# Performance work log

Hardware: AMD Instinct MI355X
Metric: run time of the kernel (lower is better)

The kernel has to match this reference:

```python
import jax, jax.numpy as jnp
import numpy as np

IN_DIM = 128
NODES = 512      # nodes per graph (equal-size graphs, as x.view(bsize,-1,in_dim) assumes)
BSIZE = 512
T = 10
ALPHA = 0.1
REG = 1e-3
EPS = 1e-5       # torch LayerNorm default eps


def _layernorm(h, g, b):
    m = jnp.mean(h, axis=-1, keepdims=True)
    v = jnp.var(h, axis=-1, keepdims=True)  # biased, like torch LayerNorm
    return (h - m) * jax.lax.rsqrt(v + EPS) * g + b


def setup_inputs() -> dict:
    key = jax.random.key(0)
    ks = jax.random.split(key, 12)
    d, h = IN_DIM, IN_DIM // 2
    x = jax.random.normal(ks[0], (BSIZE * NODES, d), dtype=jnp.float32)
    batch = jnp.repeat(jnp.arange(BSIZE, dtype=jnp.int64), NODES)
    def lin(k, fi, fo):
        bound = 1.0 / np.sqrt(fi)
        k1, k2 = jax.random.split(k)
        W = jax.random.uniform(k1, (fi, fo), jnp.float32, -bound, bound)
        b = jax.random.uniform(k2, (fo,), jnp.float32, -bound, bound)
        return W, b
    W1, b1 = lin(ks[1], 2 * d, d)
    W2, b2 = lin(ks[2], d, h)
    W3, b3 = lin(ks[3], h, 10)
    g1, be1 = jnp.ones((d,), jnp.float32), jnp.zeros((d,), jnp.float32)
    g2, be2 = jnp.ones((h,), jnp.float32), jnp.zeros((h,), jnp.float32)
    return {"x": x, "batch": batch, "W1": W1, "b1": b1, "g1": g1, "be1": be1,
            "W2": W2, "b2": b2, "g2": g2, "be2": be2, "W3": W3, "b3": b3}


def reference(x, batch, W1, b1, g1, be1, W2, b2, g2, be2, W3, b3):
    bsize = x.shape[0] // NODES  # batch ids are 0..bsize-1, NODES nodes per graph
    x3 = x.reshape(bsize, NODES, IN_DIM)

    def potential(z):  # z: [B, N, 2*d] -> [B, N, 10]
        hh = _layernorm(jnp.tanh(z @ W1 + b1), g1, be1)
        hh = _layernorm(jnp.tanh(hh @ W2 + b2), g2, be2)
        return hh @ W3 + b3

    def energy_sum(y):  # scalar: sum over graphs of per-graph energy
        yb = jnp.broadcast_to(y[:, None, :], x3.shape)
        p = potential(jnp.concatenate([x3, yb], axis=-1))
        u = jnp.mean(p * p, axis=-1).sum(axis=-1) + REG * jnp.mean(y * y, axis=-1)
        return u.sum()

    egrad = jax.grad(energy_sum)

    def step(y, _):
        g = egrad(y)
        return y - ALPHA * g, g

    y0 = jnp.zeros((bsize, IN_DIM), dtype=x.dtype)
    yT, grads = jax.lax.scan(step, y0, None, length=T)
    return yT, grads
```

## Files before the change

### kernel.cpp

```cpp
#include <hip/hip_runtime.h>


typedef __attribute__((ext_vector_type(8))) short s8v;
typedef __attribute__((ext_vector_type(4))) float f4v;

#define OFF_W1T 0
#define OFF_W1Y 67584
#define OFF_W2T 102400
#define OFF_W2B 118784
#define OFF_W3T 135168
#define OFF_W3B 137216
#define OFF_YBF 141312
#define OFF_YF  272384

static __device__ __forceinline__ unsigned short f2b(float f){
  unsigned u = __float_as_uint(f);
  u = u + 0x7FFFu + ((u >> 16) & 1u);
  return (unsigned short)(u >> 16);
}
static __device__ __forceinline__ float ftanh(float a){
  float e = __expf(2.0f * a);
  return 1.0f - __fdividef(2.0f, e + 1.0f);
}
static __device__ __forceinline__ float rsum16(float v){
  v += __shfl_xor(v, 1); v += __shfl_xor(v, 2);
  v += __shfl_xor(v, 4); v += __shfl_xor(v, 8);
  return v;
}
static __device__ __forceinline__ f4v mfma16(s8v a, s8v b, f4v c){
  return __builtin_amdgcn_mfma_f32_16x16x32_bf16(a, b, c, 0, 0, 0);
}

__global__ void prep_kernel(const float* __restrict__ W1, const float* __restrict__ W2,
                            const float* __restrict__ W3, char* __restrict__ ws){
  int tid = blockIdx.x * blockDim.x + threadIdx.x;
  int nt = gridDim.x * blockDim.x;
  unsigned short* w1t = (unsigned short*)(ws + OFF_W1T);
  for (int idx = tid; idx < 128 * 256; idx += nt){
    int n = idx >> 8, k = idx & 255;
    w1t[n * 264 + k] = f2b(W1[k * 128 + n]);
  }
  unsigned short* w1y = (unsigned short*)(ws + OFF_W1Y);
  for (int idx = tid; idx < 128 * 128; idx += nt){
    int n = idx >> 7, k = idx & 127;
    w1y[n * 136 + k] = f2b(W1[(128 + n) * 128 + k]);
  }
  unsigned short* w2t = (unsigned short*)(ws + OFF_W2T);
  for (int idx = tid; idx < 16 * 512; idx += nt){
    int f = idx >> 9, pos = idx & 511, l = pos >> 3, j = pos & 7;
    int ntile = f >> 2, kt = f & 3;
    int n = ntile * 16 + (l & 15), k = kt * 32 + (l >> 4) * 8 + j;
    w2t[idx] = f2b(W2[k * 64 + n]);
  }
  unsigned short* w2b = (unsigned short*)(ws + OFF_W2B);
  for (int idx = tid; idx < 16 * 512; idx += nt){
    int f = idx >> 9, pos = idx & 511, l = pos >> 3, j = pos & 7;
    int ntile = f >> 1, kt = f & 1;
    int n = ntile * 16 + (l & 15), k = kt * 32 + (l >> 4) * 8 + j;
    w2b[idx] = f2b(W2[n * 64 + k]);
  }
  unsigned short* w3t = (unsigned short*)(ws + OFF_W3T);
  for (int idx = tid; idx < 2 * 512; idx += nt){
    int f = idx >> 9, pos = idx & 511, l = pos >> 3, j = pos & 7;
    int n = (l & 15), k = f * 32 + (l >> 4) * 8 + j;
    w3t[idx] = (n < 10) ? f2b(W3[k * 10 + n]) : (unsigned short)0;
  }
  unsigned short* w3b = (unsigned short*)(ws + OFF_W3B);
  for (int idx = tid; idx < 4 * 512; idx += nt){
    int f = idx >> 9, pos = idx & 511, l = pos >> 3, j = pos & 7;
    int n = f * 16 + (l & 15), k = (l >> 4) * 8 + j;
    w3b[idx] = (k < 10) ? f2b(W3[n * 10 + k]) : (unsigned short)0;
  }
}

struct __align__(16) SMem {
  unsigned short w1t[128 * 264];
  unsigned short w1y[128 * 136];
  unsigned short buf1[64 * 136];
  unsigned short buf2[64 * 72];
  float red_s[64][4];
  float red_q[64][4];
  unsigned short ybuf[128];
};

__launch_bounds__(512, 2)
__global__ void node_kernel(const float* __restrict__ x,
    const float* __restrict__ b1, const float* __restrict__ g1, const float* __restrict__ be1,
    const float* __restrict__ b2, const float* __restrict__ g2, const float* __restrict__ be2,
    const float* __restrict__ b3,
    const char* __restrict__ ws, float* __restrict__ grads_t){
  __shared__ SMem sm;
  const int tid = threadIdx.x;
  const int lane = tid & 63;
  const int w  = tid >> 6;
  const int wm = w >> 2;
  const int wn = w & 3;
  const int lg = lane >> 4;
  const int lr = lane & 15;

  const unsigned short* w2t_g = (const unsigned short*)(ws + OFF_W2T);
  const unsigned short* w2b_g = (const unsigned short*)(ws + OFF_W2B);
  const unsigned short* w3t_g = (const unsigned short*)(ws + OFF_W3T);
  const unsigned short* w3b_g = (const unsigned short*)(ws + OFF_W3B);
  const unsigned short* ybf_g = (const unsigned short*)(ws + OFF_YBF);

  {
    const uint4* src = (const uint4*)(ws + OFF_W1T);
    uint4* dst = (uint4*)&sm.w1t[0];
    #pragma unroll 1
    for (int i = tid; i < (67584 + 34816) / 16; i += 512) dst[i] = src[i];
  }

  const f4v z4 = {0.f, 0.f, 0.f, 0.f};
  const s8v z8 = {0, 0, 0, 0, 0, 0, 0, 0};

  #pragma unroll 1
  for (int c = blockIdx.x; c < 4096; c += gridDim.x){
    const int graph = c >> 3;
    const int node0 = c << 6;
    if (tid < 16) ((uint4*)sm.ybuf)[tid] = ((const uint4*)(ybf_g + graph * 128))[tid];
    __syncthreads();

    f4v acc1[2][2];
    acc1[0][0]=z4; acc1[0][1]=z4; acc1[1][0]=z4; acc1[1][1]=z4;
    #pragma unroll
    for (int kt = 0; kt < 8; ++kt){
      s8v af[2];
      if (kt < 4){
        #pragma unroll
        for (int i = 0; i < 2; ++i){
          const float* p = x + (size_t)(node0 + (wm*2+i)*16 + lr) * 128 + kt*32 + lg*8;
          float4 f0 = *(const float4*)p;
          float4 f1 = *(const float4*)(p + 4);
          s8v t;
          t[0]=(short)f2b(f0.x); t[1]=(short)f2b(f0.y); t[2]=(short)f2b(f0.z); t[3]=(short)f2b(f0.w);
          t[4]=(short)f2b(f1.x); t[5]=(short)f2b(f1.y); t[6]=(short)f2b(f1.z); t[7]=(short)f2b(f1.w);
          af[i] = t;
        }
      } else {
        s8v t = *(const s8v*)&sm.ybuf[(kt-4)*32 + lg*8];
        af[0] = t; af[1] = t;
      }
      #pragma unroll
      for (int jn = 0; jn < 2; ++jn){
        s8v bf = *(const s8v*)&sm.w1t[((wn*2+jn)*16 + lr)*264 + kt*32 + lg*8];
        #pragma unroll
        for (int i = 0; i < 2; ++i)
          acc1[i][jn] = mfma16(af[i], bf, acc1[i][jn]);
      }
    }

    float tv[2][2][4], xh1[2][2][4], dd1[2][2][4], sig1[2][4];
    #pragma unroll
    for (int i = 0; i < 2; ++i)
      #pragma unroll
      for (int jn = 0; jn < 2; ++jn){
        float bb = b1[wn*32 + jn*16 + lr];
        #pragma unroll
        for (int r = 0; r < 4; ++r)
          tv[i][jn][r] = ftanh(acc1[i][jn][r] + bb);
      }
    #pragma unroll
    for (int i = 0; i < 2; ++i)
      #pragma unroll
      for (int r = 0; r < 4; ++r){
        float s = tv[i][0][r] + tv[i][1][r];
        float q = tv[i][0][r]*tv[i][0][r] + tv[i][1][r]*tv[i][1][r];
        s = rsum16(s); q = rsum16(q);
        if (lr == 0){
          int row = (wm*2+i)*16 + lg*4 + r;
          sm.red_s[row][wn] = s; sm.red_q[row][wn] = q;
        }
      }
    __syncthreads();
    #pragma unroll
    for (int i = 0; i < 2; ++i)
      #pragma unroll
      for (int r = 0; r < 4; ++r){
        int row = (wm*2+i)*16 + lg*4 + r;
        float4 ss = *(const float4*)&sm.red_s[row][0];
        float4 qq = *(const float4*)&sm.red_q[row][0];
        float S = (ss.x + ss.y) + (ss.z + ss.w);
        float Q = (qq.x + qq.y) + (qq.z + qq.w);
        float mu  = S * (1.0f/128.0f);
        float var = Q * (1.0f/128.0f) - mu*mu;
        float sg  = rsqrtf(var + 1e-5f);
        sig1[i][r] = sg;
        #pragma unroll
        for (int jn = 0; jn < 2; ++jn){
          int col = wn*32 + jn*16 + lr;
          float tt = tv[i][jn][r];
          float xh = (tt - mu) * sg;
          xh1[i][jn][r] = xh;
          dd1[i][jn][r] = 1.0f - tt*tt;
          sm.buf1[row*136 + col] = f2b(xh * g1[col] + be1[col]);
        }
      }
    __syncthreads();

    f4v acc2[2]; acc2[0]=z4; acc2[1]=z4;
    #pragma unroll
    for (int kt = 0; kt < 4; ++kt){
      s8v bf = *(const s8v*)(w2t_g + ((wn*4 + kt)*64 + lane)*8);
      #pragma unroll
      for (int i = 0; i < 2; ++i){
        s8v af = *(const s8v*)&sm.buf1[((wm*2+i)*16 + lr)*136 + kt*32 + lg*8];
        acc2[i] = mfma16(af, bf, acc2[i]);
      }
    }
    float t2[2][4], xh2[2][4], dd2[2][4], sig2[2][4];
    {
      const int col2 = wn*16 + lr;
      float bb = b2[col2];
      #pragma unroll
      for (int i = 0; i < 2; ++i)
        #pragma unroll
        for (int r = 0; r < 4; ++r)
          t2[i][r] = ftanh(acc2[i][r] + bb);
      #pragma unroll
      for (int i = 0; i < 2; ++i)
        #pragma unroll
        for (int r = 0; r < 4; ++r){
          float s = rsum16(t2[i][r]);
          float q = rsum16(t2[i][r]*t2[i][r]);
          if (lr == 0){
            int row = (wm*2+i)*16 + lg*4 + r;
            sm.red_s[row][wn] = s; sm.red_q[row][wn] = q;
          }
        }
      __syncthreads();
      #pragma unroll
      for (int i = 0; i < 2; ++i)
        #pragma unroll
        for (int r = 0; r < 4; ++r){
          int row = (wm*2+i)*16 + lg*4 + r;
          float4 ss = *(const float4*)&sm.red_s[row][0];
          float4 qq = *(const float4*)&sm.red_q[row][0];
          float S = (ss.x+ss.y)+(ss.z+ss.w);
          float Q = (qq.x+qq.y)+(qq.z+qq.w);
          float mu  = S * (1.0f/64.0f);
          float var = Q * (1.0f/64.0f) - mu*mu;
          float sg  = rsqrtf(var + 1e-5f);
          sig2[i][r] = sg;
          float tt = t2[i][r];
          float xh = (tt - mu) * sg;
          xh2[i][r] = xh; dd2[i][r] = 1.0f - tt*tt;
          sm.buf2[row*72 + col2] = f2b(xh * g2[col2] + be2[col2]);
        }
      __syncthreads();
    }

    if (wn == 0){
      f4v acc3[2]; acc3[0]=z4; acc3[1]=z4;
      #pragma unroll
      for (int kt = 0; kt < 2; ++kt){
        s8v bf = *(const s8v*)(w3t_g + (kt*64 + lane)*8);
        #pragma unroll
        for (int i = 0; i < 2; ++i){
          s8v af = *(const s8v*)&sm.buf2[((wm*2+i)*16 + lr)*72 + kt*32 + lg*8];
          acc3[i] = mfma16(af, bf, acc3[i]);
        }
      }
      float bb3 = (lr < 10) ? b3[lr] : 0.0f;
      #pragma unroll
      for (int i = 0; i < 2; ++i)
        #pragma unroll
        for (int r = 0; r < 4; ++r){
          int row = (wm*2+i)*16 + lg*4 + r;
          float p = acc3[i][r] + bb3;
          sm.buf1[row*24 + lr] = (lr < 10) ? f2b(0.2f * p) : (unsigned short)0;
        }
    }
    __syncthreads();

    f4v accb3[2]; accb3[0]=z4; accb3[1]=z4;
    {
      s8v bf = *(const s8v*)(w3b_g + (wn*64 + lane)*8);
      #pragma unroll
      for (int i = 0; i < 2; ++i){
        s8v af = z8;
        if (lg < 2) af = *(const s8v*)&sm.buf1[((wm*2+i)*16 + lr)*24 + lg*8];
        accb3[i] = mfma16(af, bf, accb3[i]);
      }
    }
    {
      const int col2 = wn*16 + lr;
      float gg = g2[col2];
      float dyv2[2][4];
      #pragma unroll
      for (int i = 0; i < 2; ++i)
        #pragma unroll
        for (int r = 0; r < 4; ++r){
          float dy = accb3[i][r] * gg;
          dyv2[i][r] = dy;
          float s1 = rsum16(dy);
          float s2 = rsum16(dy * xh2[i][r]);
          if (lr == 0){
            int row = (wm*2+i)*16 + lg*4 + r;
            sm.red_s[row][wn] = s1; sm.red_q[row][wn] = s2;
          }
        }
      __syncthreads();
      #pragma unroll
      for (int i = 0; i < 2; ++i)
        #pragma unroll
        for (int r = 0; r < 4; ++r){
          int row = (wm*2+i)*16 + lg*4 + r;
          float4 ss = *(const float4*)&sm.red_s[row][0];
          float4 qq = *(const float4*)&sm.red_q[row][0];
          float S1 = (ss.x+ss.y)+(ss.z+ss.w);
          float S2 = (qq.x+qq.y)+(qq.z+qq.w);
          float dt = sig2[i][r] * (dyv2[i][r] - S1*(1.0f/64.0f) - xh2[i][r]*S2*(1.0f/64.0f));
          sm.buf2[row*72 + col2] = f2b(dt * dd2[i][r]);
        }
      __syncthreads();
    }

    f4v accb2[2][2];
    accb2[0][0]=z4; accb2[0][1]=z4; accb2[1][0]=z4; accb2[1][1]=z4;
    #pragma unroll
    for (int kt = 0; kt < 2; ++kt){
      s8v af[2];
      #pragma unroll
      for (int i = 0; i < 2; ++i)
        af[i] = *(const s8v*)&sm.buf2[((wm*2+i)*16 + lr)*72 + kt*32 + lg*8];
      #pragma unroll
      for (int jn = 0; jn < 2; ++jn){
        s8v bf = *(const s8v*)(w2b_g + (((wn*2+jn)*2 + kt)*64 + lane)*8);
        #pragma unroll
        for (int i = 0; i < 2; ++i)
          accb2[i][jn] = mfma16(af[i], bf, accb2[i][jn]);
      }
    }
    {
      float dyv[2][2][4];
      #pragma unroll
      for (int i = 0; i < 2; ++i)
        #pragma unroll
        for (int jn = 0; jn < 2; ++jn){
          float gg = g1[wn*32 + jn*16 + lr];
          #pragma unroll
          for (int r = 0; r < 4; ++r)
            dyv[i][jn][r] = accb2[i][jn][r] * gg;
        }
      #pragma unroll
      for (int i = 0; i < 2; ++i)
        #pragma unroll
        for (int r = 0; r < 4; ++r){
          float s1 = dyv[i][0][r] + dyv[i][1][r];
          float s2 = dyv[i][0][r]*xh1[i][0][r] + dyv[i][1][r]*xh1[i][1][r];
          s1 = rsum16(s1); s2 = rsum16(s2);
          if (lr == 0){
            int row = (wm*2+i)*16 + lg*4 + r;
            sm.red_s[row][wn] = s1; sm.red_q[row][wn] = s2;
          }
        }
      __syncthreads();
      #pragma unroll
      for (int i = 0; i < 2; ++i)
        #pragma unroll
        for (int r = 0; r < 4; ++r){
          int row = (wm*2+i)*16 + lg*4 + r;
          float4 ss = *(const float4*)&sm.red_s[row][0];
          float4 qq = *(const float4*)&sm.red_q[row][0];
          float S1 = (ss.x+ss.y)+(ss.z+ss.w);
          float S2 = (qq.x+qq.y)+(qq.z+qq.w);
          #pragma unroll
          for (int jn = 0; jn < 2; ++jn){
            int col = wn*32 + jn*16 + lr;
            float dt = sig1[i][r]*(dyv[i][jn][r] - S1*(1.0f/128.0f) - xh1[i][jn][r]*S2*(1.0f/128.0f));
            sm.buf1[row*136 + col] = f2b(dt * dd1[i][jn][r]);
          }
        }
      __syncthreads();
    }

    f4v accz[2][2];
    accz[0][0]=z4; accz[0][1]=z4; accz[1][0]=z4; accz[1][1]=z4;
    #pragma unroll
    for (int kt = 0; kt < 4; ++kt){
      s8v af[2];
      #pragma unroll
      for (int i = 0; i < 2; ++i)
        af[i] = *(const s8v*)&sm.buf1[((wm*2+i)*16 + lr)*136 + kt*32 + lg*8];
      #pragma unroll
      for (int jn = 0; jn < 2; ++jn){
        s8v bf = *(const s8v*)&sm.w1y[((wn*2+jn)*16 + lr)*136 + kt*32 + lg*8];
        #pragma unroll
        for (int i = 0; i < 2; ++i)
          accz[i][jn] = mfma16(af[i], bf, accz[i][jn]);
      }
    }
    #pragma unroll
    for (int jn = 0; jn < 2; ++jn){
      float s = ((accz[0][jn][0] + accz[0][jn][1]) + (accz[0][jn][2] + accz[0][jn][3]))
              + ((accz[1][jn][0] + accz[1][jn][1]) + (accz[1][jn][2] + accz[1][jn][3]));
      s += __shfl_xor(s, 16);
      s += __shfl_xor(s, 32);
      if (lg == 0)
        atomicAdd(&grads_t[graph*128 + wn*32 + jn*16 + lr], s);
    }
  }
}

__global__ void update_kernel(char* __restrict__ ws, float* __restrict__ dout, int t){
  int idx = blockIdx.x * blockDim.x + threadIdx.x;
  float* gr = dout + 65536 + t * 65536;
  float* y  = (float*)(ws + OFF_YF);
  unsigned short* yb = (unsigned short*)(ws + OFF_YBF);
  float g = gr[idx] + 1.5625e-5f * y[idx];
  gr[idx] = g;
  float yn = y[idx] - 0.1f * g;
  y[idx] = yn;
  yb[idx] = f2b(yn);
  if (t == 9) dout[idx] = yn;
}

extern "C" void kernel_launch(void* const* d_in, const int* in_sizes, int n_in,
                              void* d_out, int out_size, void* d_ws, size_t ws_size,
                              hipStream_t stream){
  const float* x   = (const float*)d_in[0];
  const float* W1  = (const float*)d_in[2];
  const float* b1  = (const float*)d_in[3];
  const float* g1  = (const float*)d_in[4];
  const float* be1 = (const float*)d_in[5];
  const float* W2  = (const float*)d_in[6];
  const float* b2  = (const float*)d_in[7];
  const float* g2  = (const float*)d_in[8];
  const float* be2 = (const float*)d_in[9];
  const float* W3  = (const float*)d_in[10];
  const float* b3  = (const float*)d_in[11];
  float* out = (float*)d_out;
  char* ws = (char*)d_ws;

  hipMemsetAsync(ws + OFF_YBF, 0, 131072 + 262144, stream);
  hipMemsetAsync(out + 65536, 0, 10 * 65536 * sizeof(float), stream);

  prep_kernel<<<64, 256, 0, stream>>>(W1, W2, W3, ws);

  for (int t = 0; t < 10; ++t){
    node_kernel<<<256, 512, 0, stream>>>(x, b1, g1, be1, b2, g2, be2, b3,
                                         (const char*)ws, out + 65536 + t * 65536);
    update_kernel<<<256, 256, 0, stream>>>(ws, out, t);
  }
}
```

Before: 2.793 ms.

## Read W1 fragments from global in MFMA layout instead of staging in LDS

Moves the W1 weight blocks (x-part and y-part) out of shared memory. They are now pre-swizzled into per-lane MFMA fragment order in the workspace and read straight from global/L2. The LDS footprint shrinks to the small activation buffers, so launch bounds rise to 4 blocks per CU and the grid doubles to 512. This removes the per-block LDS fill of about 100KB and the per-chunk ybuf sync. In exchange every MFMA B operand becomes a global load that depends on cache hits, and a trailing __syncthreads is added per chunk.

Result: slower. 3.577 ms (+28.1%).

```diff
diff --git a/kernel.cpp b/kernel.cpp
--- a/kernel.cpp
+++ b/kernel.cpp
@@ -5,13 +5,13 @@
 typedef __attribute__((ext_vector_type(4))) float f4v;
 
 #define OFF_W1T 0
-#define OFF_W1Y 67584
-#define OFF_W2T 102400
-#define OFF_W2B 118784
-#define OFF_W3T 135168
-#define OFF_W3B 137216
-#define OFF_YBF 141312
-#define OFF_YF  272384
+#define OFF_W1Y 65536
+#define OFF_W2T 98304
+#define OFF_W2B 114688
+#define OFF_W3T 131072
+#define OFF_W3B 133120
+#define OFF_YBF 137216
+#define OFF_YF  268288
 
 static __device__ __forceinline__ unsigned short f2b(float f){
   unsigned u = __float_as_uint(f);
@@ -36,14 +36,18 @@
   int tid = blockIdx.x * blockDim.x + threadIdx.x;
   int nt = gridDim.x * blockDim.x;
   unsigned short* w1t = (unsigned short*)(ws + OFF_W1T);
-  for (int idx = tid; idx < 128 * 256; idx += nt){
-    int n = idx >> 8, k = idx & 255;
-    w1t[n * 264 + k] = f2b(W1[k * 128 + n]);
+  for (int idx = tid; idx < 64 * 512; idx += nt){
+    int f = idx >> 9, pos = idx & 511, l = pos >> 3, j = pos & 7;
+    int ntile = f >> 3, kt = f & 7;
+    int n = ntile * 16 + (l & 15), k = kt * 32 + (l >> 4) * 8 + j;
+    w1t[idx] = f2b(W1[k * 128 + n]);
   }
   unsigned short* w1y = (unsigned short*)(ws + OFF_W1Y);
-  for (int idx = tid; idx < 128 * 128; idx += nt){
-    int n = idx >> 7, k = idx & 127;
-    w1y[n * 136 + k] = f2b(W1[(128 + n) * 128 + k]);
+  for (int idx = tid; idx < 32 * 512; idx += nt){
+    int f = idx >> 9, pos = idx & 511, l = pos >> 3, j = pos & 7;
+    int ntile = f >> 2, kt = f & 3;
+    int n = ntile * 16 + (l & 15), k = kt * 32 + (l >> 4) * 8 + j;
+    w1y[idx] = f2b(W1[(128 + n) * 128 + k]);
   }
   unsigned short* w2t = (unsigned short*)(ws + OFF_W2T);
   for (int idx = tid; idx < 16 * 512; idx += nt){
@@ -74,16 +78,13 @@
 }
 
 struct __align__(16) SMem {
-  unsigned short w1t[128 * 264];
-  unsigned short w1y[128 * 136];
   unsigned short buf1[64 * 136];
   unsigned short buf2[64 * 72];
   float red_s[64][4];
   float red_q[64][4];
-  unsigned short ybuf[128];
 };
 
-__launch_bounds__(512, 2)
+__launch_bounds__(512, 4)
 __global__ void node_kernel(const float* __restrict__ x,
     const float* __restrict__ b1, const float* __restrict__ g1, const float* __restrict__ be1,
     const float* __restrict__ b2, const float* __restrict__ g2, const float* __restrict__ be2,
@@ -98,19 +99,14 @@
   const int lg = lane >> 4;
   const int lr = lane & 15;
 
+  const unsigned short* w1t_g = (const unsigned short*)(ws + OFF_W1T);
+  const unsigned short* w1y_g = (const unsigned short*)(ws + OFF_W1Y);
   const unsigned short* w2t_g = (const unsigned short*)(ws + OFF_W2T);
   const unsigned short* w2b_g = (const unsigned short*)(ws + OFF_W2B);
   const unsigned short* w3t_g = (const unsigned short*)(ws + OFF_W3T);
   const unsigned short* w3b_g = (const unsigned short*)(ws + OFF_W3B);
   const unsigned short* ybf_g = (const unsigned short*)(ws + OFF_YBF);
 
-  {
-    const uint4* src = (const uint4*)(ws + OFF_W1T);
-    uint4* dst = (uint4*)&sm.w1t[0];
-    #pragma unroll 1
-    for (int i = tid; i < (67584 + 34816) / 16; i += 512) dst[i] = src[i];
-  }
-
   const f4v z4 = {0.f, 0.f, 0.f, 0.f};
   const s8v z8 = {0, 0, 0, 0, 0, 0, 0, 0};
 
@@ -118,8 +114,6 @@
   for (int c = blockIdx.x; c < 4096; c += gridDim.x){
     const int graph = c >> 3;
     const int node0 = c << 6;
-    if (tid < 16) ((uint4*)sm.ybuf)[tid] = ((const uint4*)(ybf_g + graph * 128))[tid];
-    __syncthreads();
 
     f4v acc1[2][2];
     acc1[0][0]=z4; acc1[0][1]=z4; acc1[1][0]=z4; acc1[1][1]=z4;
@@ -138,12 +132,12 @@
           af[i] = t;
         }
       } else {
-        s8v t = *(const s8v*)&sm.ybuf[(kt-4)*32 + lg*8];
+        s8v t = *(const s8v*)(ybf_g + graph*128 + (kt-4)*32 + lg*8);
         af[0] = t; af[1] = t;
       }
       #pragma unroll
       for (int jn = 0; jn < 2; ++jn){
-        s8v bf = *(const s8v*)&sm.w1t[((wn*2+jn)*16 + lr)*264 + kt*32 + lg*8];
+        s8v bf = *(const s8v*)(w1t_g + (((wn*2+jn)*8 + kt)*64 + lane)*8);
         #pragma unroll
         for (int i = 0; i < 2; ++i)
           acc1[i][jn] = mfma16(af[i], bf, acc1[i][jn]);
@@ -385,7 +379,7 @@
         af[i] = *(const s8v*)&sm.buf1[((wm*2+i)*16 + lr)*136 + kt*32 + lg*8];
       #pragma unroll
       for (int jn = 0; jn < 2; ++jn){
-        s8v bf = *(const s8v*)&sm.w1y[((wn*2+jn)*16 + lr)*136 + kt*32 + lg*8];
+        s8v bf = *(const s8v*)(w1y_g + (((wn*2+jn)*4 + kt)*64 + lane)*8);
         #pragma unroll
         for (int i = 0; i < 2; ++i)
           accz[i][jn] = mfma16(af[i], bf, accz[i][jn]);
@@ -400,6 +394,7 @@
       if (lg == 0)
         atomicAdd(&grads_t[graph*128 + wn*32 + jn*16 + lr], s);
     }
+    __syncthreads();
   }
 }
 
@@ -439,7 +434,7 @@
   prep_kernel<<<64, 256, 0, stream>>>(W1, W2, W3, ws);
 
   for (int t = 0; t < 10; ++t){
-    node_kernel<<<256, 512, 0, stream>>>(x, b1, g1, be1, b2, g2, be2, b3,
+    node_kernel<<<512, 512, 0, stream>>>(x, b1, g1, be1, b2, g2, be2, b3,
                                          (const char*)ws, out + 65536 + t * 65536);
     update_kernel<<<256, 256, 0, stream>>>(ws, out, t);
   }
```
